# Kernel tuning notes

Hardware: AMD Instinct MI355X
Metric: run time of the kernel (lower is better)

Reference implementation:

```python
import jax, jax.numpy as jnp
import numpy as np

WIN = 9  # window size per spatial dim (default [9,9,9] for 3D)


def _window_sum(x):
    # Depthwise conv with an all-ones [9,9,9] kernel, stride 1, zero pad 4
    # == sliding-window box sum. lax.reduce_window is the efficient, exact form.
    pad = WIN // 2
    return jax.lax.reduce_window(
        x, 0.0, jax.lax.add,
        window_dimensions=(1, 1, WIN, WIN, WIN),
        window_strides=(1, 1, 1, 1, 1),
        padding=((0, 0), (0, 0), (pad, pad), (pad, pad), (pad, pad)),
    )


def setup_inputs() -> dict:
    key = jax.random.key(0)
    k1, k2 = jax.random.split(key)
    shape = (2, 1, 160, 160, 160)  # [B, C, D, H, W]
    y_true = jax.random.normal(k1, shape, dtype=jnp.float32)
    y_pred = jax.random.normal(k2, shape, dtype=jnp.float32)
    return {"y_true": y_true, "y_pred": y_pred}


def reference(y_true, y_pred):
    Ii, Ji = y_true, y_pred
    win_size = jnp.asarray(WIN ** 3, dtype=Ii.dtype)  # 729

    I2 = Ii * Ii
    J2 = Ji * Ji
    IJ = Ii * Ji

    I_sum = _window_sum(Ii)
    J_sum = _window_sum(Ji)
    I2_sum = _window_sum(I2)
    J2_sum = _window_sum(J2)
    IJ_sum = _window_sum(IJ)

    u_I = I_sum / win_size
    u_J = J_sum / win_size

    cross = IJ_sum - u_J * I_sum - u_I * J_sum + u_I * u_J * win_size
    I_var = I2_sum - 2.0 * u_I * I_sum + u_I * u_I * win_size
    J_var = J2_sum - 2.0 * u_J * J_sum + u_J * u_J * win_size

    cc = cross * cross / (I_var * J_var + 1e-05)
    # mean over spatial dims [2,3,4] -> [B,C], then mean -> scalar
    return (1.0 - jnp.mean(cc, axis=(2, 3, 4))).mean()
```

## Files before the change

### kernel.cpp

```cpp
#include <hip/hip_runtime.h>


typedef float floatx2 __attribute__((ext_vector_type(2)));

constexpr int W = 160, H = 160, D = 160;
constexpr int SLICE = W * H;
constexpr int NVOX  = W * H * D;
constexpr int BATCH = 2;
constexpr int FROW  = 5 * W;
constexpr float RW  = 1.0f / 729.0f;

constexpr int TPB_P = 400;
constexpr int XT    = 80;
constexpr int NXT   = W / XT;
constexpr int CZ    = 80;
constexpr int NCZ   = D / CZ;
constexpr int ZS    = CZ + 8;
constexpr int NUNITS = ZS * 10;
constexpr int NBLK_P = BATCH * H * NXT * NCZ;

constexpr int TPB_Y = 256;
constexpr int XGY   = W / 8;
constexpr int CHY   = 2, NCHY = H / CHY;
constexpr int NTH_Y = BATCH * D * NCHY * XGY;
constexpr int NBLK_Y = NTH_Y / TPB_Y;

__device__ inline unsigned int pk4(float a, float b, float c, float d) {
    unsigned int u = 0;
    u = __builtin_amdgcn_cvt_pk_fp8_f32(a, b, u, false);
    u = __builtin_amdgcn_cvt_pk_fp8_f32(c, d, u, true);
    return u;
}
__device__ inline void up4(unsigned int v, float* o) {
    floatx2 t;
    t = __builtin_amdgcn_cvt_pk_f32_fp8(v, false); o[0] = t[0]; o[1] = t[1];
    t = __builtin_amdgcn_cvt_pk_f32_fp8(v, true);  o[2] = t[0]; o[3] = t[1];
}
__device__ inline void up8(uint2 v, float* o) {
    up4(v.x, o); up4(v.y, o + 4);
}

__global__ __launch_bounds__(TPB_P) void pass_pzx(const float* __restrict__ I,
                                                  const float* __restrict__ J,
                                                  unsigned char* __restrict__ outA) {
    __shared__ unsigned char xw[5][ZS][XT];

    int blk = blockIdx.x;
    int zc = blk % NCZ;
    int xt = (blk / NCZ) % NXT;
    int y  = (blk / (NCZ * NXT)) % H;
    int b  = blk / (NCZ * NXT * H);
    int tx0 = xt * XT;
    int zbase = zc * CZ - 4;
    const float* Ib = I + (size_t)b * NVOX + y * W;
    const float* Jb = J + (size_t)b * NVOX + y * W;

    const float4 Z4 = make_float4(0.f, 0.f, 0.f, 0.f);
    for (int u = threadIdx.x; u < NUNITS; u += TPB_P) {
        int zs = u / 10;
        int xu = u % 10;
        int gxs = tx0 + xu * 8;
        int gz = zbase + zs;
        float a[16], c[16];
        if (gz >= 0 && gz < D) {
            const float* ip = Ib + (size_t)gz * SLICE + gxs;
            const float* jp = Jb + (size_t)gz * SLICE + gxs;
            float4 A0 = (gxs >= 4)     ? *(const float4*)(ip - 4) : Z4;
            float4 A1 = *(const float4*)(ip);
            float4 A2 = *(const float4*)(ip + 4);
            float4 A3 = (gxs + 11 < W) ? *(const float4*)(ip + 8) : Z4;
            float4 C0 = (gxs >= 4)     ? *(const float4*)(jp - 4) : Z4;
            float4 C1 = *(const float4*)(jp);
            float4 C2 = *(const float4*)(jp + 4);
            float4 C3 = (gxs + 11 < W) ? *(const float4*)(jp + 8) : Z4;
            float at[16] = {A0.x,A0.y,A0.z,A0.w, A1.x,A1.y,A1.z,A1.w,
                            A2.x,A2.y,A2.z,A2.w, A3.x,A3.y,A3.z,A3.w};
            float ct[16] = {C0.x,C0.y,C0.z,C0.w, C1.x,C1.y,C1.z,C1.w,
                            C2.x,C2.y,C2.z,C2.w, C3.x,C3.y,C3.z,C3.w};
#pragma unroll
            for (int k = 0; k < 16; ++k) { a[k] = at[k]; c[k] = ct[k]; }
        } else {
#pragma unroll
            for (int k = 0; k < 16; ++k) { a[k] = 0.f; c[k] = 0.f; }
        }
#pragma unroll
        for (int f = 0; f < 5; ++f) {
            float v[16];
#pragma unroll
            for (int k = 0; k < 16; ++k) {
                float x = a[k], yv = c[k];
                v[k] = (f == 0) ? x : (f == 1) ? yv :
                       (f == 2) ? x * x : (f == 3) ? yv * yv : x * yv;
            }
            float P[16];
            P[0] = v[0];
#pragma unroll
            for (int k = 1; k < 16; ++k) P[k] = P[k - 1] + v[k];
            float w[8];
            w[0] = P[8];
#pragma unroll
            for (int j = 1; j < 8; ++j) w[j] = P[j + 8] - P[j - 1];
            uint2 pk;
            pk.x = pk4(w[0], w[1], w[2], w[3]);
            pk.y = pk4(w[4], w[5], w[6], w[7]);
            *(uint2*)&xw[f][zs][xu * 8] = pk;
        }
    }

    __syncthreads();

    {
        int xg = threadIdx.x % 20;
        int zl = threadIdx.x / 20;
        int x0l = xg * 4;
        int zo0 = zl * 4;

        float acc[5][4];
#pragma unroll
        for (int f = 0; f < 5; ++f)
#pragma unroll
            for (int i = 0; i < 4; ++i) acc[f][i] = 0.f;

#pragma unroll
        for (int k = 0; k < 9; ++k) {
#pragma unroll
            for (int f = 0; f < 5; ++f) {
                unsigned int v = *(const unsigned int*)&xw[f][zo0 + k][x0l];
                float u[4]; up4(v, u);
                acc[f][0] += u[0]; acc[f][1] += u[1];
                acc[f][2] += u[2]; acc[f][3] += u[3];
            }
        }

        int gz0 = zc * CZ + zo0;
        unsigned char* op = outA + ((size_t)(b * D + gz0) * H + y) * FROW + tx0 + x0l;
#pragma unroll
        for (int q = 0; q < 4; ++q) {
#pragma unroll
            for (int f = 0; f < 5; ++f)
                *(unsigned int*)(op + f * W) =
                    pk4(acc[f][0], acc[f][1], acc[f][2], acc[f][3]);
            if (q < 3) {
#pragma unroll
                for (int f = 0; f < 5; ++f) {
                    unsigned int ve = *(const unsigned int*)&xw[f][zo0 + 9 + q][x0l];
                    unsigned int vl = *(const unsigned int*)&xw[f][zo0 + q][x0l];
                    float ue[4], ul[4];
                    up4(ve, ue); up4(vl, ul);
                    acc[f][0] += ue[0] - ul[0]; acc[f][1] += ue[1] - ul[1];
                    acc[f][2] += ue[2] - ul[2]; acc[f][3] += ue[3] - ul[3];
                }
                op += (size_t)H * FROW;
            }
        }
    }
}

__global__ __launch_bounds__(TPB_Y) void pass_y(const unsigned char* __restrict__ A,
                                                double* __restrict__ partials) {
    int tid = threadIdx.x;
    int t = blockIdx.x * TPB_Y + tid;
    int xg = t % XGY;
    int tup = t / XGY;
    int yc = tup % NCHY;
    int z  = (tup / NCHY) % D;
    int b  = tup / (NCHY * D);
    int x0 = xg * 8;
    const unsigned char* __restrict__ base =
        A + (size_t)(b * D + z) * H * FROW + x0;
    int y0 = yc * CHY;

    float s[5][8];
#pragma unroll
    for (int f = 0; f < 5; ++f)
#pragma unroll
        for (int i = 0; i < 8; ++i) s[f][i] = 0.f;

    int ylo = y0 - 4 < 0 ? 0 : y0 - 4;
    int yhi = y0 + 4 > H - 1 ? H - 1 : y0 + 4;
    for (int yy = ylo; yy <= yhi; ++yy) {
        const unsigned char* rp = base + (size_t)yy * FROW;
#pragma unroll
        for (int f = 0; f < 5; ++f) {
            uint2 v = *(const uint2*)(rp + f * W);
            float u[8]; up8(v, u);
#pragma unroll
            for (int i = 0; i < 8; ++i) s[f][i] += u[i];
        }
    }

    double acc = 0.0;
#pragma unroll
    for (int dy = 0; dy < CHY; ++dy) {
        int ye = y0 + dy + 5, yl = y0 + dy - 4;
        bool he = ye < H, hl = yl >= 0;
        uint2 pe[5], pl[5];
        const unsigned char* pre = base + (size_t)(he ? ye : 0) * FROW;
        const unsigned char* prl = base + (size_t)(hl ? yl : 0) * FROW;
#pragma unroll
        for (int f = 0; f < 5; ++f) {
            pe[f] = he ? *(const uint2*)(pre + f * W) : make_uint2(0u, 0u);
            pl[f] = hl ? *(const uint2*)(prl + f * W) : make_uint2(0u, 0u);
        }

        float rowcc = 0.f;
#pragma unroll
        for (int i = 0; i < 8; ++i) {
            float Is = s[0][i], Js = s[1][i];
            float I2s = s[2][i], J2s = s[3][i], IJs = s[4][i];
            float tI = RW * Is;
            float cross = __builtin_fmaf(-tI, Js, IJs);
            float Iv    = __builtin_fmaf(-tI, Is, I2s);
            float Jv    = __builtin_fmaf(-(RW * Js), Js, J2s);
            float den   = __builtin_fmaf(Iv, Jv, 1e-5f);
            rowcc = __builtin_fmaf(cross * cross, __builtin_amdgcn_rcpf(den), rowcc);
        }
        acc += (double)rowcc;

#pragma unroll
        for (int f = 0; f < 5; ++f) {
            float ue[8], ul[8];
            up8(pe[f], ue); up8(pl[f], ul);
#pragma unroll
            for (int i = 0; i < 8; ++i) s[f][i] += ue[i] - ul[i];
        }
    }

#pragma unroll
    for (int off = 32; off > 0; off >>= 1) acc += __shfl_down(acc, off);
    __shared__ double sm[TPB_Y / 64];
    if ((tid & 63) == 0) sm[tid >> 6] = acc;
    __syncthreads();
    if (tid == 0) {
        double tt = 0.0;
#pragma unroll
        for (int i = 0; i < TPB_Y / 64; ++i) tt += sm[i];
        partials[blockIdx.x] = tt;
    }
}

__global__ __launch_bounds__(256) void finalize(const double* __restrict__ p,
                                                float* __restrict__ out) {
    double v = 0.0;
    for (int i = threadIdx.x; i < NBLK_Y; i += 256) v += p[i];
#pragma unroll
    for (int off = 32; off > 0; off >>= 1) v += __shfl_down(v, off);
    __shared__ double sm[4];
    int lane = threadIdx.x & 63, wid = threadIdx.x >> 6;
    if (lane == 0) sm[wid] = v;
    __syncthreads();
    if (threadIdx.x == 0) {
        double tt = 0.0;
#pragma unroll
        for (int i = 0; i < 4; ++i) tt += sm[i];
        out[0] = (float)(1.0 - tt / (double)((double)BATCH * (double)NVOX));
    }
}

extern "C" void kernel_launch(void* const* d_in, const int* in_sizes, int n_in,
                              void* d_out, int out_size, void* d_ws, size_t ws_size,
                              hipStream_t stream) {
    const float* I = (const float*)d_in[0];
    const float* J = (const float*)d_in[1];
    float* out = (float*)d_out;

    size_t bufsz = ((size_t)BATCH * 5 * NVOX + 255) / 256 * 256;
    unsigned char* bufA = (unsigned char*)d_ws;
    double* partials = (double*)(bufA + bufsz);

    pass_pzx<<<NBLK_P, TPB_P, 0, stream>>>(I, J, bufA);
    pass_y<<<NBLK_Y, TPB_Y, 0, stream>>>(bufA, partials);
    finalize<<<1, 256, 0, stream>>>(partials, out);
}
```

Baseline: 60.23 us.

## Stage y-window rows in shared memory for the y-pass reduction

The y-pass kernel now has each block cooperatively load a 48-row halo tile (40 output rows plus 8 halo rows) of the fp8 packed 5-field buffer into LDS. Threads then compute their 9-row window sums and the two output rows from LDS instead of re-reading overlapping rows from global memory. This targets the roughly 5x redundant global/L2 reads of halo rows in the previous per-thread approach. It costs a __syncthreads, about 38KB of LDS per block that may limit occupancy, and 48 of the 448 threads sit idle during compute.

```diff
diff --git a/kernel.cpp b/kernel.cpp
--- a/kernel.cpp
+++ b/kernel.cpp
@@ -19,11 +19,12 @@
 constexpr int NUNITS = ZS * 10;
 constexpr int NBLK_P = BATCH * H * NXT * NCZ;
 
-constexpr int TPB_Y = 256;
-constexpr int XGY   = W / 8;
-constexpr int CHY   = 2, NCHY = H / CHY;
-constexpr int NTH_Y = BATCH * D * NCHY * XGY;
-constexpr int NBLK_Y = NTH_Y / TPB_Y;
+constexpr int TPB_Y = 448;
+constexpr int YQ    = 40;
+constexpr int NYQ   = H / YQ;
+constexpr int YR    = YQ + 8;
+constexpr int NBLK_Y = BATCH * D * NYQ;
+constexpr int LDW   = YR * FROW / 16;
 
 __device__ inline unsigned int pk4(float a, float b, float c, float d) {
     unsigned int u = 0;
@@ -156,79 +157,89 @@
     }
 }
 
-__global__ __launch_bounds__(TPB_Y) void pass_y(const unsigned char* __restrict__ A,
-                                                double* __restrict__ partials) {
+__global__ __launch_bounds__(TPB_Y) void pass_y2(const unsigned char* __restrict__ A,
+                                                 double* __restrict__ partials) {
+    __shared__ unsigned char rows[YR * FROW];
+    __shared__ double sm[TPB_Y / 64];
+
+    int blk = blockIdx.x;
+    int yq = blk % NYQ;
+    int z  = (blk / NYQ) % D;
+    int b  = blk / (NYQ * D);
+    int y0 = yq * YQ;
     int tid = threadIdx.x;
-    int t = blockIdx.x * TPB_Y + tid;
-    int xg = t % XGY;
-    int tup = t / XGY;
-    int yc = tup % NCHY;
-    int z  = (tup / NCHY) % D;
-    int b  = tup / (NCHY * D);
-    int x0 = xg * 8;
-    const unsigned char* __restrict__ base =
-        A + (size_t)(b * D + z) * H * FROW + x0;
-    int y0 = yc * CHY;
-
-    float s[5][8];
-#pragma unroll
-    for (int f = 0; f < 5; ++f)
-#pragma unroll
-        for (int i = 0; i < 8; ++i) s[f][i] = 0.f;
-
-    int ylo = y0 - 4 < 0 ? 0 : y0 - 4;
-    int yhi = y0 + 4 > H - 1 ? H - 1 : y0 + 4;
-    for (int yy = ylo; yy <= yhi; ++yy) {
-        const unsigned char* rp = base + (size_t)yy * FROW;
-#pragma unroll
-        for (int f = 0; f < 5; ++f) {
-            uint2 v = *(const uint2*)(rp + f * W);
-            float u[8]; up8(v, u);
-#pragma unroll
-            for (int i = 0; i < 8; ++i) s[f][i] += u[i];
-        }
-    }
+    const unsigned char* __restrict__ src =
+        A + ((size_t)(b * D + z) * H) * FROW;
+
+    for (int i = tid; i < LDW; i += TPB_Y) {
+        int off = i * 16;
+        int r = off / FROW;
+        int gy = y0 - 4 + r;
+        uint4 v = make_uint4(0u, 0u, 0u, 0u);
+        if (gy >= 0 && gy < H)
+            v = *(const uint4*)(src + (size_t)gy * FROW + (off % FROW));
+        *(uint4*)&rows[off] = v;
+    }
+    __syncthreads();
 
     double acc = 0.0;
-#pragma unroll
-    for (int dy = 0; dy < CHY; ++dy) {
-        int ye = y0 + dy + 5, yl = y0 + dy - 4;
-        bool he = ye < H, hl = yl >= 0;
-        uint2 pe[5], pl[5];
-        const unsigned char* pre = base + (size_t)(he ? ye : 0) * FROW;
-        const unsigned char* prl = base + (size_t)(hl ? yl : 0) * FROW;
-#pragma unroll
-        for (int f = 0; f < 5; ++f) {
-            pe[f] = he ? *(const uint2*)(pre + f * W) : make_uint2(0u, 0u);
-            pl[f] = hl ? *(const uint2*)(prl + f * W) : make_uint2(0u, 0u);
-        }
-
-        float rowcc = 0.f;
-#pragma unroll
-        for (int i = 0; i < 8; ++i) {
-            float Is = s[0][i], Js = s[1][i];
-            float I2s = s[2][i], J2s = s[3][i], IJs = s[4][i];
-            float tI = RW * Is;
-            float cross = __builtin_fmaf(-tI, Js, IJs);
-            float Iv    = __builtin_fmaf(-tI, Is, I2s);
-            float Jv    = __builtin_fmaf(-(RW * Js), Js, J2s);
-            float den   = __builtin_fmaf(Iv, Jv, 1e-5f);
-            rowcc = __builtin_fmaf(cross * cross, __builtin_amdgcn_rcpf(den), rowcc);
-        }
-        acc += (double)rowcc;
-
-#pragma unroll
-        for (int f = 0; f < 5; ++f) {
-            float ue[8], ul[8];
-            up8(pe[f], ue); up8(pl[f], ul);
-#pragma unroll
-            for (int i = 0; i < 8; ++i) s[f][i] += ue[i] - ul[i];
+    if (tid < 400) {
+        int xg = tid % 20;
+        int ys = tid / 20;
+        int rbase = ys * 2;
+        int x8 = xg * 8;
+
+        float s[5][8];
+#pragma unroll
+        for (int f = 0; f < 5; ++f)
+#pragma unroll
+            for (int i = 0; i < 8; ++i) s[f][i] = 0.f;
+
+#pragma unroll
+        for (int t = 0; t < 9; ++t) {
+            const unsigned char* rp = &rows[(rbase + t) * FROW + x8];
+#pragma unroll
+            for (int f = 0; f < 5; ++f) {
+                uint2 v = *(const uint2*)(rp + f * W);
+                float u[8]; up8(v, u);
+#pragma unroll
+                for (int i = 0; i < 8; ++i) s[f][i] += u[i];
+            }
+        }
+
+#pragma unroll
+        for (int o = 0; o < 2; ++o) {
+            float rowcc = 0.f;
+#pragma unroll
+            for (int i = 0; i < 8; ++i) {
+                float Is = s[0][i], Js = s[1][i];
+                float I2s = s[2][i], J2s = s[3][i], IJs = s[4][i];
+                float tI = RW * Is;
+                float cross = __builtin_fmaf(-tI, Js, IJs);
+                float Iv    = __builtin_fmaf(-tI, Is, I2s);
+                float Jv    = __builtin_fmaf(-(RW * Js), Js, J2s);
+                float den   = __builtin_fmaf(Iv, Jv, 1e-5f);
+                rowcc = __builtin_fmaf(cross * cross, __builtin_amdgcn_rcpf(den), rowcc);
+            }
+            acc += (double)rowcc;
+            if (o == 0) {
+                const unsigned char* re = &rows[(rbase + 9) * FROW + x8];
+                const unsigned char* rl = &rows[rbase * FROW + x8];
+#pragma unroll
+                for (int f = 0; f < 5; ++f) {
+                    uint2 ve = *(const uint2*)(re + f * W);
+                    uint2 vl = *(const uint2*)(rl + f * W);
+                    float ue[8], ul[8];
+                    up8(ve, ue); up8(vl, ul);
+#pragma unroll
+                    for (int i = 0; i < 8; ++i) s[f][i] += ue[i] - ul[i];
+                }
+            }
         }
     }
 
 #pragma unroll
     for (int off = 32; off > 0; off >>= 1) acc += __shfl_down(acc, off);
-    __shared__ double sm[TPB_Y / 64];
     if ((tid & 63) == 0) sm[tid >> 6] = acc;
     __syncthreads();
     if (tid == 0) {
@@ -269,6 +280,6 @@
     double* partials = (double*)(bufA + bufsz);
 
     pass_pzx<<<NBLK_P, TPB_P, 0, stream>>>(I, J, bufA);
-    pass_y<<<NBLK_Y, TPB_Y, 0, stream>>>(bufA, partials);
+    pass_y2<<<NBLK_Y, TPB_Y, 0, stream>>>(bufA, partials);
     finalize<<<1, 256, 0, stream>>>(partials, out);
 }
```

Result: no change. 59.64 us (median of 3 runs) (-1.0%).
